# Kernel optimization log

Measured on AMD Instinct MI355X. Metric: run time of the kernel, lower is better.

Reference implementation:

```python
import jax, jax.numpy as jnp
import numpy as np

B, N, M = 4, 2048, 2048
DIM, DIM_KEYS, DIM_OUT = 512, 512, 512
HEADS, DIM_HEAD = 8, 64
INNER = HEADS * DIM_HEAD


def setup_inputs() -> dict:
    key = jax.random.key(0)
    ks = jax.random.split(key, 9)
    x = jax.random.normal(ks[0], (B, N, DIM), dtype=jnp.float32)
    context = jax.random.normal(ks[1], (B, M, DIM_KEYS), dtype=jnp.float32)
    mask = jax.random.randint(ks[2], (B, N), 0, 2).astype(bool)
    context_mask = jax.random.randint(ks[3], (B, M), 0, 2).astype(bool)
    Wq = jax.random.normal(ks[4], (DIM, INNER), dtype=jnp.float32) * 0.02
    Wkv = jax.random.normal(ks[5], (DIM_KEYS, 2 * INNER), dtype=jnp.float32) * 0.02
    Wo = jax.random.normal(ks[6], (INNER, DIM_OUT), dtype=jnp.float32) * 0.02
    bo = jnp.zeros((DIM_OUT,), dtype=jnp.float32)
    null_key = jax.random.normal(ks[7], (DIM_HEAD,), dtype=jnp.float32)
    null_value = jax.random.normal(ks[8], (DIM_HEAD,), dtype=jnp.float32)
    return {"x": x, "context": context, "mask": mask, "context_mask": context_mask,
            "Wq": Wq, "Wkv": Wkv, "Wo": Wo, "bo": bo,
            "null_key": null_key, "null_value": null_value}


def reference(x, context, mask, context_mask, Wq, Wkv, Wo, bo, null_key, null_value):
    b, n, _ = x.shape
    m = context.shape[1]
    h, dh = HEADS, DIM_HEAD
    scale = dh ** -0.5

    # projections -> [b, h, n, dh]
    q = (x @ Wq).reshape(b, n, h, dh).transpose(0, 2, 1, 3)
    kv = context @ Wkv  # [b, m, 2*inner]
    k, v = jnp.split(kv, 2, axis=-1)
    k = k.reshape(b, m, h, dh).transpose(0, 2, 1, 3)
    v = v.reshape(b, m, h, dh).transpose(0, 2, 1, 3)

    # prepend null key/value token -> j = m + 1
    nk = jnp.broadcast_to(null_key, (b, h, 1, dh))
    nv = jnp.broadcast_to(null_value, (b, h, 1, dh))
    k = jnp.concatenate([nk, k], axis=2)
    v = jnp.concatenate([nv, v], axis=2)

    # qk activation (tanh) BEFORE the dot product
    q = jnp.tanh(q)
    k = jnp.tanh(k)

    sim = jnp.einsum('bhid,bhjd->bhij', q, k) * scale  # [b,h,n,m+1]

    # null token is always attendable -> pad context mask with True
    cm = jnp.pad(context_mask, ((0, 0), (1, 0)), constant_values=True)
    full_mask = mask[:, None, :, None] & cm[:, None, None, :]
    neg = -jnp.finfo(sim.dtype).max
    sim = jnp.where(full_mask, sim, neg)

    attn = jax.nn.softmax(sim, axis=-1)
    out = jnp.einsum('bhij,bhjd->bhid', attn, v)
    out = out.transpose(0, 2, 1, 3).reshape(b, n, h * dh)
    return out @ Wo + bo
```

## Files before the change

### kernel.cpp

```cpp
#include <hip/hip_runtime.h>
#include <math.h>

#define BB 4
#define NN 2048
#define MM 2048
#define HEADS 8
#define DH 64

typedef _Float16 f16;
typedef _Float16 f16x4 __attribute__((ext_vector_type(4)));
typedef _Float16 f16x8 __attribute__((ext_vector_type(8)));
typedef float f32x4 __attribute__((ext_vector_type(4)));
typedef unsigned short ushort;

#define LOG2E 1.44269504088896f
#define QSCALE (0.125f * LOG2E)

#if __has_builtin(__builtin_amdgcn_exp2f)
#define EXP2(x) __builtin_amdgcn_exp2f(x)
#else
#define EXP2(x) exp2f(x)
#endif

__device__ __forceinline__ f16x4 pk4(float a, float b, float c, float d) {
#if __has_builtin(__builtin_amdgcn_cvt_pkrtz)
    auto t0 = __builtin_amdgcn_cvt_pkrtz(a, b);
    auto t1 = __builtin_amdgcn_cvt_pkrtz(c, d);
    f16x4 r;
    r[0] = t0[0]; r[1] = t0[1]; r[2] = t1[0]; r[3] = t1[1];
    return r;
#else
    f16x4 r = {(f16)a, (f16)b, (f16)c, (f16)d};
    return r;
#endif
}

__device__ __forceinline__ void gl16(const void* g, void* l) {
    __builtin_amdgcn_global_load_lds(
        (const __attribute__((address_space(1))) unsigned int*)g,
        (__attribute__((address_space(3))) unsigned int*)l, 16, 0, 0);
}

__global__ void wprep_k(const float* __restrict__ Wq, const float* __restrict__ Wkv,
                        const float* __restrict__ Wo,
                        f16* __restrict__ wq16, f16* __restrict__ wkv16,
                        f16* __restrict__ woh, f16* __restrict__ wol)
{
    __shared__ f16 S0[64 * 36], S1[64 * 36];
    const int tid = threadIdx.x;
    const int bid = blockIdx.x;
    const int K = 512;
    const float* W; int N; f16* T16; f16 *Th, *Tl; int id;
    if (bid < 128)      { W = Wq;  N = 512;  T16 = wq16;  Th = 0; Tl = 0; id = bid; }
    else if (bid < 384) { W = Wkv; N = 1024; T16 = wkv16; Th = 0; Tl = 0; id = bid - 128; }
    else                { W = Wo;  N = 512;  T16 = 0; Th = woh; Tl = wol; id = bid - 384; }
    const int k0 = (id & 15) * 32, n0 = (id >> 4) * 64;
    const int kr = tid >> 3, nc = (tid & 7) * 8;
    float4 v0 = *(const float4*)(W + (size_t)(k0 + kr) * N + n0 + nc);
    float4 v1 = *(const float4*)(W + (size_t)(k0 + kr) * N + n0 + nc + 4);
    float e[8] = {v0.x, v0.y, v0.z, v0.w, v1.x, v1.y, v1.z, v1.w};
    const int n = tid >> 2, kc = (tid & 3) * 8;
    if (T16) {
#pragma unroll
        for (int j = 0; j < 8; j++) S0[(nc + j) * 36 + kr] = (f16)e[j];
        __syncthreads();
        *(uint4*)(T16 + (size_t)(n0 + n) * K + k0 + kc) = *(const uint4*)(S0 + n * 36 + kc);
    } else {
#pragma unroll
        for (int j = 0; j < 8; j++) {
            f16 h = (f16)e[j];
            S0[(nc + j) * 36 + kr] = h;
            S1[(nc + j) * 36 + kr] = (f16)(e[j] - (float)h);
        }
        __syncthreads();
        *(uint4*)(Th + (size_t)(n0 + n) * K + k0 + kc) = *(const uint4*)(S0 + n * 36 + kc);
        *(uint4*)(Tl + (size_t)(n0 + n) * K + k0 + kc) = *(const uint4*)(S1 + n * 36 + kc);
    }
}

__global__ void xprep_k(const float* __restrict__ x, const float* __restrict__ ctx,
                        f16* __restrict__ xf, f16* __restrict__ cf)
{
    const size_t S = (size_t)BB * NN * 512;
    const size_t i = ((size_t)blockIdx.x * 256 + threadIdx.x) * 8;
    const float* src = (i < S) ? x + i : ctx + (i - S);
    f16* dst         = (i < S) ? xf + i : cf + (i - S);
    float4 v0 = *(const float4*)(src);
    float4 v1 = *(const float4*)(src + 4);
    f16x8 o;
    o[0] = (f16)v0.x; o[1] = (f16)v0.y; o[2] = (f16)v0.z; o[3] = (f16)v0.w;
    o[4] = (f16)v1.x; o[5] = (f16)v1.y; o[6] = (f16)v1.z; o[7] = (f16)v1.w;
    *(f16x8*)dst = o;
}

__launch_bounds__(256, 3)
__global__ void proj_k(const f16* __restrict__ xf, const f16* __restrict__ cf,
                       const f16* __restrict__ wq16, const f16* __restrict__ wkv16,
                       f16* __restrict__ qws, f16* __restrict__ kws, f16* __restrict__ vt)
{
    __shared__ __align__(16) char smem[32768];

    const int tid  = threadIdx.x;
    const int wave = tid >> 6, lane = tid & 63;
    const int l15  = lane & 15, quad = lane >> 4;
    const int by = blockIdx.y;
    const int isQ = (by < 4);
    const f16* A16 = isQ ? xf : cf;
    const f16* Bt  = isQ ? wq16 : wkv16;
    const int c0 = (isQ ? by : by - 4) * 128;
    const size_t r0 = (size_t)blockIdx.x * 128;
    const int K = 512;

    const int row0 = wave * 32 + (lane >> 2);
    const int swc  = (lane & 3) ^ ((lane >> 3) & 3);
    const char* aP0 = (const char*)(A16 + (r0 + row0) * K)       + swc * 16;
    const char* aP1 = (const char*)(A16 + (r0 + row0 + 16) * K)  + swc * 16;
    const char* bP0 = (const char*)(Bt + (size_t)(c0 + row0) * K)      + swc * 16;
    const char* bP1 = (const char*)(Bt + (size_t)(c0 + row0 + 16) * K) + swc * 16;
    char* aD = smem + wave * 2048;
    char* bD = smem + 8192 + wave * 2048;

    gl16(aP0, aD); gl16(aP1, aD + 1024);
    gl16(bP0, bD); gl16(bP1, bD + 1024);
    aP0 += 64; aP1 += 64; bP0 += 64; bP1 += 64;

    const int fsw = ((quad ^ ((l15 >> 1) & 3)) << 4);
    const int aoff0 = (wave * 32 + l15) * 64 + fsw;
    const int aoff1 = (wave * 32 + 16 + l15) * 64 + fsw;

    f32x4 acc[2][8] = {};
    __syncthreads();

    int buf = 0;
    for (int t = 0; t < 16; t++) {
        const int nb = (buf ^ 1) * 16384;
        if (t < 15) {
            gl16(aP0, aD + nb); gl16(aP1, aD + nb + 1024);
            gl16(bP0, bD + nb); gl16(bP1, bD + nb + 1024);
            aP0 += 64; aP1 += 64; bP0 += 64; bP1 += 64;
        }
        const char* sA = smem + buf * 16384;
        const char* sB = sA + 8192;

        f16x8 a[2];
        a[0] = *(const f16x8*)(sA + aoff0);
        a[1] = *(const f16x8*)(sA + aoff1);
#pragma unroll
        for (int half = 0; half < 2; half++) {
            f16x8 b[4];
#pragma unroll
            for (int c = 0; c < 4; c++)
                b[c] = *(const f16x8*)(sB + ((half * 4 + c) * 16 + l15) * 64 + fsw);
#pragma unroll
            for (int rt = 0; rt < 2; rt++)
#pragma unroll
                for (int c = 0; c < 4; c++)
                    acc[rt][half * 4 + c] = __builtin_amdgcn_mfma_f32_16x16x32_f16(
                        a[rt], b[c], acc[rt][half * 4 + c], 0, 0, 0);
        }
        __syncthreads();
        buf ^= 1;
    }

    const int b    = (int)(r0 >> 11);
    const int rloc = ((int)(r0 & 2047)) + wave * 32;

#pragma unroll
    for (int rt = 0; rt < 2; rt++)
#pragma unroll
        for (int ct = 0; ct < 8; ct++) {
            const int col = c0 + ct * 16 + l15;
            if (isQ || col < 512) {
                const int h = (col >> 6) & 7;
                const int d = col & 63;
                f16* dst = isQ ? qws : kws;
                const float sc = isQ ? QSCALE : 1.0f;
#pragma unroll
                for (int reg = 0; reg < 4; reg++) {
                    const int nn = rloc + rt * 16 + quad * 4 + reg;
                    dst[(((size_t)b * 8 + h) * 2048 + nn) * 64 + d] =
                        (f16)(tanhf(acc[rt][ct][reg]) * sc);
                }
            } else {
                const int c = col - 512;
                const int h = c >> 6;
                const int d = c & 63;
                const int m0 = rloc + rt * 16 + quad * 4;
                f16x4 pk;
#pragma unroll
                for (int reg = 0; reg < 4; reg++) pk[reg] = (f16)acc[rt][ct][reg];
                *(f16x4*)(vt + (((size_t)b * 8 + h) * 64 + d) * 2048 + m0) = pk;
            }
        }
}

__launch_bounds__(256, 4)
__global__ void attn_k(const f16* __restrict__ qws, const f16* __restrict__ kws,
                       const f16* __restrict__ vtws,
                       const int* __restrict__ mask, const int* __restrict__ cmask,
                       const float* __restrict__ nk, const float* __restrict__ nv,
                       f16* __restrict__ Opf, float* __restrict__ lp)
{
    __shared__ __align__(16) char smem[32768];

    const int tid  = threadIdx.x;
    const int wave = tid >> 6, lane = tid & 63;
    const int l15  = lane & 15, quad = lane >> 4;
    const int bh = blockIdx.x, b = bh >> 3, h = bh & 7;
    const int q0 = blockIdx.y * 128 + wave * 32;
    const int jh = blockIdx.z;
    const int jbeg = jh << 9, jend = jbeg + 512;

    const f16* kg0 = kws + (size_t)bh * MM * DH;
    const f16* vg0 = vtws + (size_t)bh * DH * MM;

    const int lrow = lane >> 3;
    const int lsw  = ((lane & 7) ^ lrow) << 4;
    const char* kP = (const char*)kg0 + (size_t)(jbeg + wave * 16 + lrow) * 128 + lsw;
    const char* vP = (const char*)vg0 + (size_t)(wave * 16 + lrow) * 4096
                   + (size_t)jbeg * 2 + lsw;
    char* kD = smem + wave * 2048;
    char* vD = smem + 8192 + wave * 2048;

    gl16(kP,         kD);
    gl16(kP + 1024,  kD + 1024);
    gl16(vP,         vD);
    gl16(vP + 32768, vD + 1024);
    kP += 8192; vP += 128;

    f16x8 qf[2][2];
    const f16* qbase = qws + ((size_t)bh * NN + q0) * DH;
#pragma unroll
    for (int rt = 0; rt < 2; rt++)
#pragma unroll
        for (int ks = 0; ks < 2; ks++)
            qf[rt][ks] = *(const f16x8*)(qbase + (rt * 16 + l15) * DH + ks * 32 + quad * 8);

    int rowOk[2];
#pragma unroll
    for (int rt = 0; rt < 2; rt++)
        rowOk[rt] = mask[(size_t)b * NN + q0 + rt * 16 + l15];

    float pnull[2] = {0.0f, 0.0f};
    if (jh == 0) {
        float pn[2] = {0.f, 0.f};
#pragma unroll
        for (int ks = 0; ks < 2; ks++)
#pragma unroll
            for (int t = 0; t < 8; t++) {
                const float nkt = tanhf(nk[ks * 32 + quad * 8 + t]);
                pn[0] += (float)qf[0][ks][t] * nkt;
                pn[1] += (float)qf[1][ks][t] * nkt;
            }
#pragma unroll
        for (int rt = 0; rt < 2; rt++) {
            pn[rt] += __shfl_xor(pn[rt], 16);
            pn[rt] += __shfl_xor(pn[rt], 32);
            pnull[rt] = rowOk[rt] ? EXP2(pn[rt]) : 1.0f;
        }
    }
    float negsel[2];
#pragma unroll
    for (int rt = 0; rt < 2; rt++) {
        negsel[rt] = rowOk[rt] ? -1.0e30f : 0.0f;
        if (!rowOk[rt]) {
            const f16x8 zz = {(f16)0, (f16)0, (f16)0, (f16)0, (f16)0, (f16)0, (f16)0, (f16)0};
            qf[rt][0] = zz; qf[rt][1] = zz;
        }
    }

    f32x4 acc[2][4];
    f32x4 accl[2];
#pragma unroll
    for (int rt = 0; rt < 2; rt++)
#pragma unroll
        for (int reg = 0; reg < 4; reg++) {
            const float pr = __shfl(pnull[rt], quad * 4 + reg, 16);
            accl[rt][reg] = pr;
#pragma unroll
            for (int ds = 0; ds < 4; ds++)
                acc[rt][ds][reg] = pr * nv[ds * 16 + l15];
        }

    const f16x4 vone = {(f16)1, (f16)1, (f16)1, (f16)1};
    const int kxor = l15 & 7;

    __syncthreads();

    int buf = 0;
    for (int jc = jbeg; jc < jend; jc += 64) {
        int4 cmv[4];
#pragma unroll
        for (int jj = 0; jj < 4; jj++)
            cmv[jj] = *(const int4*)(cmask + (size_t)b * MM + jc + jj * 16 + quad * 4);

        if (jc + 64 < jend) {
            const int bo = (buf ^ 1) << 14;
            gl16(kP,         kD + bo);
            gl16(kP + 1024,  kD + bo + 1024);
            gl16(vP,         vD + bo);
            gl16(vP + 32768, vD + bo + 1024);
            kP += 8192; vP += 128;
        }

        const char* sKb = smem + (buf << 14);
        const char* sVb = sKb + 8192;

        f32x4 st[2][4];
#pragma unroll
        for (int rt = 0; rt < 2; rt++)
#pragma unroll
            for (int jj = 0; jj < 4; jj++) {
                st[rt][jj][0] = cmv[jj].x ? 0.0f : negsel[rt];
                st[rt][jj][1] = cmv[jj].y ? 0.0f : negsel[rt];
                st[rt][jj][2] = cmv[jj].z ? 0.0f : negsel[rt];
                st[rt][jj][3] = cmv[jj].w ? 0.0f : negsel[rt];
            }

#pragma unroll
        for (int ks = 0; ks < 2; ks++) {
            f16x8 kb[4];
#pragma unroll
            for (int jj = 0; jj < 4; jj++)
                kb[jj] = *(const f16x8*)(sKb + (jj * 16 + l15) * 128
                                             + (((ks * 4 + quad) ^ kxor) << 4));
#pragma unroll
            for (int rt = 0; rt < 2; rt++)
#pragma unroll
                for (int jj = 0; jj < 4; jj++)
                    st[rt][jj] = __builtin_amdgcn_mfma_f32_16x16x32_f16(
                        kb[jj], qf[rt][ks], st[rt][jj], 0, 0, 0);
        }

        f16x4 pa[2][4];
#pragma unroll
        for (int rt = 0; rt < 2; rt++)
#pragma unroll
            for (int jj = 0; jj < 4; jj++)
                pa[rt][jj] = pk4(EXP2(st[rt][jj][0]), EXP2(st[rt][jj][1]),
                                 EXP2(st[rt][jj][2]), EXP2(st[rt][jj][3]));

#pragma unroll
        for (int jj = 0; jj < 4; jj++) {
            f16x4 vb[4];
#pragma unroll
            for (int ds = 0; ds < 4; ds++)
                vb[ds] = *(const f16x4*)(sVb + (ds * 16 + l15) * 128
                                             + (((jj * 2 + (quad >> 1)) ^ kxor) << 4)
                                             + ((quad & 1) << 3));
#pragma unroll
            for (int rt = 0; rt < 2; rt++) {
#pragma unroll
                for (int ds = 0; ds < 4; ds++)
                    acc[rt][ds] = __builtin_amdgcn_mfma_f32_16x16x16f16(
                        pa[rt][jj], vb[ds], acc[rt][ds], 0, 0, 0);
                accl[rt] = __builtin_amdgcn_mfma_f32_16x16x16f16(
                    pa[rt][jj], vone, accl[rt], 0, 0, 0);
            }
        }

        __syncthreads();
        buf ^= 1;
    }

#pragma unroll
    for (int rt = 0; rt < 2; rt++) {
        float inv[4];
#pragma unroll
        for (int reg = 0; reg < 4; reg++)
            inv[reg] = 1.0f / fmaxf(accl[rt][reg], 1e-35f);
#pragma unroll
        for (int ds = 0; ds < 4; ds++)
#pragma unroll
            for (int reg = 0; reg < 4; reg++) {
                const int r = q0 + rt * 16 + quad * 4 + reg;
                Opf[((size_t)jh * 8192 + b * 2048 + r) * 512 + h * 64 + ds * 16 + l15] =
                    (f16)(acc[rt][ds][reg] * inv[reg]);
            }
    }
    if (l15 == 0) {
#pragma unroll
        for (int rt = 0; rt < 2; rt++)
#pragma unroll
            for (int reg = 0; reg < 4; reg++)
                lp[((size_t)jh * 32 + bh) * 2048 + q0 + rt * 16 + quad * 4 + reg] =
                    accl[rt][reg];
    }
}

__global__ void merge_k(const f16* __restrict__ Opf, const float* __restrict__ lp,
                        f16* __restrict__ of16)
{
    const int i = blockIdx.x * 256 + threadIdx.x;
    const int row = i >> 7;
    const int c4  = i & 127;
    const int b = row >> 11, n = row & 2047, h = c4 >> 4;
    float w[4], den = 0.f;
#pragma unroll
    for (int jh = 0; jh < 4; jh++) {
        w[jh] = lp[((size_t)jh * 32 + b * 8 + h) * 2048 + n];
        den += w[jh];
    }
    const float inv = 1.0f / den;
    float v0 = 0, v1 = 0, v2 = 0, v3 = 0;
#pragma unroll
    for (int jh = 0; jh < 4; jh++) {
        f16x4 o = *(const f16x4*)(Opf + ((size_t)jh * 8192 + row) * 512 + c4 * 4);
        v0 += (float)o[0] * w[jh];
        v1 += (float)o[1] * w[jh];
        v2 += (float)o[2] * w[jh];
        v3 += (float)o[3] * w[jh];
    }
    f16x4 r = pk4(v0 * inv, v1 * inv, v2 * inv, v3 * inv);
    *(f16x4*)(of16 + (size_t)row * 512 + c4 * 4) = r;
}

__launch_bounds__(256, 3)
__global__ void mgemm2(const f16* __restrict__ A, const f16* __restrict__ Bh,
                       const f16* __restrict__ Bl,
                       float* __restrict__ o32, const float* __restrict__ bias,
                       int K)
{
    __shared__ __align__(16) char smem[49152];

    const int tid  = threadIdx.x;
    const int wave = tid >> 6, lane = tid & 63;
    const int l15  = lane & 15, quad = lane >> 4;
    const size_t r0 = (size_t)blockIdx.x * 128;
    const int c0 = blockIdx.y * 128;

    const int row0 = wave * 32 + (lane >> 2);
    const int swc  = (lane & 3) ^ ((lane >> 3) & 3);
    const char* aP0 = (const char*)(A + (r0 + row0) * K)       + swc * 16;
    const char* aP1 = (const char*)(A + (r0 + row0 + 16) * K)  + swc * 16;
    const char* hP0 = (const char*)(Bh + (size_t)(c0 + row0) * K)      + swc * 16;
    const char* hP1 = (const char*)(Bh + (size_t)(c0 + row0 + 16) * K) + swc * 16;
    const char* lP0 = (const char*)(Bl + (size_t)(c0 + row0) * K)      + swc * 16;
    const char* lP1 = (const char*)(Bl + (size_t)(c0 + row0 + 16) * K) + swc * 16;
    char* aD = smem + wave * 2048;
    char* hD = smem + 8192 + wave * 2048;
    char* lD = smem + 16384 + wave * 2048;

    gl16(aP0, aD); gl16(aP1, aD + 1024);
    gl16(hP0, hD); gl16(hP1, hD + 1024);
    gl16(lP0, lD); gl16(lP1, lD + 1024);
    aP0 += 64; aP1 += 64; hP0 += 64; hP1 += 64; lP0 += 64; lP1 += 64;

    const int fsw = ((quad ^ ((l15 >> 1) & 3)) << 4);
    const int aoff0 = (wave * 32 + l15) * 64 + fsw;
    const int aoff1 = (wave * 32 + 16 + l15) * 64 + fsw;

    f32x4 acc[2][8] = {};
    __syncthreads();

    int buf = 0;
    const int NT = K / 32;
    for (int t = 0; t < NT; t++) {
        const int nb = (buf ^ 1) * 24576;
        if (t < NT - 1) {
            gl16(aP0, aD + nb); gl16(aP1, aD + nb + 1024);
            gl16(hP0, hD + nb); gl16(hP1, hD + nb + 1024);
            gl16(lP0, lD + nb); gl16(lP1, lD + nb + 1024);
            aP0 += 64; aP1 += 64; hP0 += 64; hP1 += 64; lP0 += 64; lP1 += 64;
        }
        const char* sA = smem + buf * 24576;
        const char* sH = sA + 8192;
        const char* sL = sA + 16384;

        f16x8 a[2];
        a[0] = *(const f16x8*)(sA + aoff0);
        a[1] = *(const f16x8*)(sA + aoff1);
#pragma unroll
        for (int half = 0; half < 2; half++) {
#pragma unroll
            for (int c = 0; c < 4; c++) {
                const int ct = half * 4 + c;
                const int boff = (ct * 16 + l15) * 64 + fsw;
                f16x8 bh = *(const f16x8*)(sH + boff);
                f16x8 bl = *(const f16x8*)(sL + boff);
#pragma unroll
                for (int rt = 0; rt < 2; rt++) {
                    acc[rt][ct] = __builtin_amdgcn_mfma_f32_16x16x32_f16(
                        a[rt], bh, acc[rt][ct], 0, 0, 0);
                    acc[rt][ct] = __builtin_amdgcn_mfma_f32_16x16x32_f16(
                        a[rt], bl, acc[rt][ct], 0, 0, 0);
                }
            }
        }
        __syncthreads();
        buf ^= 1;
    }

#pragma unroll
    for (int rt = 0; rt < 2; rt++)
#pragma unroll
        for (int ct = 0; ct < 8; ct++) {
            const int col = c0 + ct * 16 + l15;
            const float bv = bias[col];
#pragma unroll
            for (int reg = 0; reg < 4; reg++) {
                const size_t row = r0 + wave * 32 + rt * 16 + quad * 4 + reg;
                o32[row * 512 + col] = acc[rt][ct][reg] + bv;
            }
        }
}

extern "C" void kernel_launch(void* const* d_in, const int* in_sizes, int n_in,
                              void* d_out, int out_size, void* d_ws, size_t ws_size,
                              hipStream_t stream)
{
    const float* x    = (const float*)d_in[0];
    const float* ctx  = (const float*)d_in[1];
    const int*   mask = (const int*)d_in[2];
    const int*   cmsk = (const int*)d_in[3];
    const float* Wq   = (const float*)d_in[4];
    const float* Wkv  = (const float*)d_in[5];
    const float* Wo   = (const float*)d_in[6];
    const float* bo   = (const float*)d_in[7];
    const float* nk   = (const float*)d_in[8];
    const float* nv   = (const float*)d_in[9];
    float* out = (float*)d_out;

    const size_t S = (size_t)BB * HEADS * NN * DH;

    f16* qws = (f16*)d_ws;
    f16* kws = qws + S;
    f16* vt  = kws + S;
    f16* wq16  = vt + S;
    f16* wkv16 = wq16 + 512 * 512;
    f16* woh = wkv16 + 512 * 1024;
    f16* wol = woh + 512 * 512;
    float* lp = (float*)(wol + 512 * 512);
    f16* Opf = (f16*)(lp + 4 * 32 * 2048);
    f16* of16 = qws;
    f16* xf16 = Opf;
    f16* cf16 = xf16 + (size_t)BB * NN * 512;

    wprep_k<<<512, 256, 0, stream>>>(Wq, Wkv, Wo, wq16, wkv16, woh, wol);
    xprep_k<<<4096, 256, 0, stream>>>(x, ctx, xf16, cf16);
    proj_k<<<dim3(64, 12), 256, 0, stream>>>(xf16, cf16, wq16, wkv16, qws, kws, vt);
    attn_k<<<dim3(32, 16, 4), 256, 0, stream>>>(qws, kws, vt, mask, cmsk, nk, nv, Opf, lp);
    merge_k<<<4096, 256, 0, stream>>>(Opf, lp, of16);
    mgemm2<<<dim3(64, 4), 256, 0, stream>>>(of16, woh, wol, out, bo, 512);
}
```

Measured before the change: 199.2 us.

## Fuse fp32-to-fp16 input conversion into projection GEMM; halve output GEMM tile width

Removes the separate xprep kernel that converted x and context to fp16. The projection GEMM now loads the fp32 rows straight into shared memory with a swizzled layout and converts them to fp16 when building the MFMA A fragments. This saves one kernel launch and one write-plus-read of the fp16 copy, but doubles the A bytes staged per tile and raises shared memory to 48KB. Separately, the output GEMM uses 64-wide column tiles with a grid of twice as many blocks and a launch bound of 4, to give more parallelism and occupancy.

Measured after the change: 190.1 us. 4.6% less time.

```diff
diff --git a/kernel.cpp b/kernel.cpp
--- a/kernel.cpp
+++ b/kernel.cpp
@@ -78,73 +78,75 @@
     }
 }
 
-__global__ void xprep_k(const float* __restrict__ x, const float* __restrict__ ctx,
-                        f16* __restrict__ xf, f16* __restrict__ cf)
-{
-    const size_t S = (size_t)BB * NN * 512;
-    const size_t i = ((size_t)blockIdx.x * 256 + threadIdx.x) * 8;
-    const float* src = (i < S) ? x + i : ctx + (i - S);
-    f16* dst         = (i < S) ? xf + i : cf + (i - S);
-    float4 v0 = *(const float4*)(src);
-    float4 v1 = *(const float4*)(src + 4);
-    f16x8 o;
-    o[0] = (f16)v0.x; o[1] = (f16)v0.y; o[2] = (f16)v0.z; o[3] = (f16)v0.w;
-    o[4] = (f16)v1.x; o[5] = (f16)v1.y; o[6] = (f16)v1.z; o[7] = (f16)v1.w;
-    *(f16x8*)dst = o;
-}
-
 __launch_bounds__(256, 3)
-__global__ void proj_k(const f16* __restrict__ xf, const f16* __restrict__ cf,
+__global__ void proj_k(const float* __restrict__ x, const float* __restrict__ ctx,
                        const f16* __restrict__ wq16, const f16* __restrict__ wkv16,
                        f16* __restrict__ qws, f16* __restrict__ kws, f16* __restrict__ vt)
 {
-    __shared__ __align__(16) char smem[32768];
+    __shared__ __align__(16) char smem[49152];
 
     const int tid  = threadIdx.x;
     const int wave = tid >> 6, lane = tid & 63;
     const int l15  = lane & 15, quad = lane >> 4;
     const int by = blockIdx.y;
     const int isQ = (by < 4);
-    const f16* A16 = isQ ? xf : cf;
+    const float* A32 = isQ ? x : ctx;
     const f16* Bt  = isQ ? wq16 : wkv16;
     const int c0 = (isQ ? by : by - 4) * 128;
     const size_t r0 = (size_t)blockIdx.x * 128;
     const int K = 512;
 
-    const int row0 = wave * 32 + (lane >> 2);
-    const int swc  = (lane & 3) ^ ((lane >> 3) & 3);
-    const char* aP0 = (const char*)(A16 + (r0 + row0) * K)       + swc * 16;
-    const char* aP1 = (const char*)(A16 + (r0 + row0 + 16) * K)  + swc * 16;
-    const char* bP0 = (const char*)(Bt + (size_t)(c0 + row0) * K)      + swc * 16;
-    const char* bP1 = (const char*)(Bt + (size_t)(c0 + row0 + 16) * K) + swc * 16;
-    char* aD = smem + wave * 2048;
-    char* bD = smem + 8192 + wave * 2048;
-
-    gl16(aP0, aD); gl16(aP1, aD + 1024);
-    gl16(bP0, bD); gl16(bP1, bD + 1024);
-    aP0 += 64; aP1 += 64; bP0 += 64; bP1 += 64;
-
+    const int alr = lane >> 3;
+    const int asw = (lane & 7) ^ alr;
+    const char* aP = (const char*)(A32 + (r0 + wave * 32 + alr) * K) + asw * 16;
+    const int blr = lane >> 2;
+    const int bsw = (lane & 3) ^ ((lane >> 3) & 3);
+    const char* bP = (const char*)(Bt + (size_t)(c0 + wave * 32 + blr) * K) + bsw * 16;
+    char* aD = smem + wave * 4096;
+    char* bD = smem + 16384 + wave * 2048;
+
+    gl16(aP,          aD);
+    gl16(aP + 16384,  aD + 1024);
+    gl16(aP + 32768,  aD + 2048);
+    gl16(aP + 49152,  aD + 3072);
+    gl16(bP,          bD);
+    gl16(bP + 16384,  bD + 1024);
+    aP += 128; bP += 64;
+
+    const int ax  = l15 & 7;
     const int fsw = ((quad ^ ((l15 >> 1) & 3)) << 4);
-    const int aoff0 = (wave * 32 + l15) * 64 + fsw;
-    const int aoff1 = (wave * 32 + 16 + l15) * 64 + fsw;
+    const int arow0 = (wave * 32 + l15) * 128;
+    const int ac0 = (((2 * quad) ^ ax) << 4);
 
     f32x4 acc[2][8] = {};
     __syncthreads();
 
     int buf = 0;
     for (int t = 0; t < 16; t++) {
-        const int nb = (buf ^ 1) * 16384;
+        const int nb = (buf ^ 1) * 24576;
         if (t < 15) {
-            gl16(aP0, aD + nb); gl16(aP1, aD + nb + 1024);
-            gl16(bP0, bD + nb); gl16(bP1, bD + nb + 1024);
-            aP0 += 64; aP1 += 64; bP0 += 64; bP1 += 64;
-        }
-        const char* sA = smem + buf * 16384;
-        const char* sB = sA + 8192;
+            gl16(aP,          aD + nb);
+            gl16(aP + 16384,  aD + nb + 1024);
+            gl16(aP + 32768,  aD + nb + 2048);
+            gl16(aP + 49152,  aD + nb + 3072);
+            gl16(bP,          bD + nb);
+            gl16(bP + 16384,  bD + nb + 1024);
+            aP += 128; bP += 64;
+        }
+        const char* sA = smem + buf * 24576;
+        const char* sB = sA + 16384;
 
         f16x8 a[2];
-        a[0] = *(const f16x8*)(sA + aoff0);
-        a[1] = *(const f16x8*)(sA + aoff1);
+#pragma unroll
+        for (int rt = 0; rt < 2; rt++) {
+            const int ab = arow0 + rt * 2048;
+            f32x4 lo = *(const f32x4*)(sA + ab + ac0);
+            f32x4 hi = *(const f32x4*)(sA + ab + (ac0 ^ 16));
+            a[rt][0] = (f16)lo[0]; a[rt][1] = (f16)lo[1];
+            a[rt][2] = (f16)lo[2]; a[rt][3] = (f16)lo[3];
+            a[rt][4] = (f16)hi[0]; a[rt][5] = (f16)hi[1];
+            a[rt][6] = (f16)hi[2]; a[rt][7] = (f16)hi[3];
+        }
 #pragma unroll
         for (int half = 0; half < 2; half++) {
             f16x8 b[4];
@@ -415,76 +417,71 @@
     *(f16x4*)(of16 + (size_t)row * 512 + c4 * 4) = r;
 }
 
-__launch_bounds__(256, 3)
+__launch_bounds__(256, 4)
 __global__ void mgemm2(const f16* __restrict__ A, const f16* __restrict__ Bh,
                        const f16* __restrict__ Bl,
                        float* __restrict__ o32, const float* __restrict__ bias,
                        int K)
 {
-    __shared__ __align__(16) char smem[49152];
+    __shared__ __align__(16) char smem[32768];
 
     const int tid  = threadIdx.x;
     const int wave = tid >> 6, lane = tid & 63;
     const int l15  = lane & 15, quad = lane >> 4;
     const size_t r0 = (size_t)blockIdx.x * 128;
-    const int c0 = blockIdx.y * 128;
-
-    const int row0 = wave * 32 + (lane >> 2);
-    const int swc  = (lane & 3) ^ ((lane >> 3) & 3);
-    const char* aP0 = (const char*)(A + (r0 + row0) * K)       + swc * 16;
-    const char* aP1 = (const char*)(A + (r0 + row0 + 16) * K)  + swc * 16;
-    const char* hP0 = (const char*)(Bh + (size_t)(c0 + row0) * K)      + swc * 16;
-    const char* hP1 = (const char*)(Bh + (size_t)(c0 + row0 + 16) * K) + swc * 16;
-    const char* lP0 = (const char*)(Bl + (size_t)(c0 + row0) * K)      + swc * 16;
-    const char* lP1 = (const char*)(Bl + (size_t)(c0 + row0 + 16) * K) + swc * 16;
+    const int c0 = blockIdx.y * 64;
+
+    const int blr = lane >> 2;
+    const int bsw = (lane & 3) ^ ((lane >> 3) & 3);
+    const char* aP = (const char*)(A + (r0 + wave * 32 + blr) * K) + bsw * 16;
+    const char* hP = (const char*)(Bh + (size_t)(c0 + wave * 16 + blr) * K) + bsw * 16;
+    const char* lP = (const char*)(Bl + (size_t)(c0 + wave * 16 + blr) * K) + bsw * 16;
     char* aD = smem + wave * 2048;
-    char* hD = smem + 8192 + wave * 2048;
-    char* lD = smem + 16384 + wave * 2048;
-
-    gl16(aP0, aD); gl16(aP1, aD + 1024);
-    gl16(hP0, hD); gl16(hP1, hD + 1024);
-    gl16(lP0, lD); gl16(lP1, lD + 1024);
-    aP0 += 64; aP1 += 64; hP0 += 64; hP1 += 64; lP0 += 64; lP1 += 64;
+    char* hD = smem + 8192 + wave * 1024;
+    char* lD = smem + 12288 + wave * 1024;
+
+    gl16(aP,          aD);
+    gl16(aP + 16384,  aD + 1024);
+    gl16(hP,          hD);
+    gl16(lP,          lD);
+    aP += 64; hP += 64; lP += 64;
 
     const int fsw = ((quad ^ ((l15 >> 1) & 3)) << 4);
     const int aoff0 = (wave * 32 + l15) * 64 + fsw;
-    const int aoff1 = (wave * 32 + 16 + l15) * 64 + fsw;
-
-    f32x4 acc[2][8] = {};
+    const int aoff1 = aoff0 + 16 * 64;
+
+    f32x4 acc[2][4] = {};
     __syncthreads();
 
     int buf = 0;
     const int NT = K / 32;
     for (int t = 0; t < NT; t++) {
-        const int nb = (buf ^ 1) * 24576;
+        const int nb = (buf ^ 1) * 16384;
         if (t < NT - 1) {
-            gl16(aP0, aD + nb); gl16(aP1, aD + nb + 1024);
-            gl16(hP0, hD + nb); gl16(hP1, hD + nb + 1024);
-            gl16(lP0, lD + nb); gl16(lP1, lD + nb + 1024);
-            aP0 += 64; aP1 += 64; hP0 += 64; hP1 += 64; lP0 += 64; lP1 += 64;
-        }
-        const char* sA = smem + buf * 24576;
+            gl16(aP,          aD + nb);
+            gl16(aP + 16384,  aD + nb + 1024);
+            gl16(hP,          hD + nb);
+            gl16(lP,          lD + nb);
+            aP += 64; hP += 64; lP += 64;
+        }
+        const char* sA = smem + buf * 16384;
         const char* sH = sA + 8192;
-        const char* sL = sA + 16384;
+        const char* sL = sA + 12288;
 
         f16x8 a[2];
         a[0] = *(const f16x8*)(sA + aoff0);
         a[1] = *(const f16x8*)(sA + aoff1);
 #pragma unroll
-        for (int half = 0; half < 2; half++) {
-#pragma unroll
-            for (int c = 0; c < 4; c++) {
-                const int ct = half * 4 + c;
-                const int boff = (ct * 16 + l15) * 64 + fsw;
-                f16x8 bh = *(const f16x8*)(sH + boff);
-                f16x8 bl = *(const f16x8*)(sL + boff);
-#pragma unroll
-                for (int rt = 0; rt < 2; rt++) {
-                    acc[rt][ct] = __builtin_amdgcn_mfma_f32_16x16x32_f16(
-                        a[rt], bh, acc[rt][ct], 0, 0, 0);
-                    acc[rt][ct] = __builtin_amdgcn_mfma_f32_16x16x32_f16(
-                        a[rt], bl, acc[rt][ct], 0, 0, 0);
-                }
+        for (int ct = 0; ct < 4; ct++) {
+            const int boff = (ct * 16 + l15) * 64 + fsw;
+            f16x8 bh = *(const f16x8*)(sH + boff);
+            f16x8 bl = *(const f16x8*)(sL + boff);
+#pragma unroll
+            for (int rt = 0; rt < 2; rt++) {
+                acc[rt][ct] = __builtin_amdgcn_mfma_f32_16x16x32_f16(
+                    a[rt], bh, acc[rt][ct], 0, 0, 0);
+                acc[rt][ct] = __builtin_amdgcn_mfma_f32_16x16x32_f16(
+                    a[rt], bl, acc[rt][ct], 0, 0, 0);
             }
         }
         __syncthreads();
@@ -494,7 +491,7 @@
 #pragma unroll
     for (int rt = 0; rt < 2; rt++)
 #pragma unroll
-        for (int ct = 0; ct < 8; ct++) {
+        for (int ct = 0; ct < 4; ct++) {
             const int col = c0 + ct * 16 + l15;
             const float bv = bias[col];
 #pragma unroll
@@ -533,13 +530,10 @@
     float* lp = (float*)(wol + 512 * 512);
     f16* Opf = (f16*)(lp + 4 * 32 * 2048);
     f16* of16 = qws;
-    f16* xf16 = Opf;
-    f16* cf16 = xf16 + (size_t)BB * NN * 512;
 
     wprep_k<<<512, 256, 0, stream>>>(Wq, Wkv, Wo, wq16, wkv16, woh, wol);
-    xprep_k<<<4096, 256, 0, stream>>>(x, ctx, xf16, cf16);
-    proj_k<<<dim3(64, 12), 256, 0, stream>>>(xf16, cf16, wq16, wkv16, qws, kws, vt);
+    proj_k<<<dim3(64, 12), 256, 0, stream>>>(x, ctx, wq16, wkv16, qws, kws, vt);
     attn_k<<<dim3(32, 16, 4), 256, 0, stream>>>(qws, kws, vt, mask, cmsk, nk, nv, Opf, lp);
     merge_k<<<4096, 256, 0, stream>>>(Opf, lp, of16);
-    mgemm2<<<dim3(64, 4), 256, 0, stream>>>(of16, woh, wol, out, bo, 512);
-}
+    mgemm2<<<dim3(64, 8), 256, 0, stream>>>(of16, woh, wol, out, bo, 512);
+}
```
